# Performance work log

Hardware: AMD Instinct MI355X
Metric: run time of the kernel (lower is better)

The kernel has to match this reference:

```python
import jax, jax.numpy as jnp
import numpy as np

B, C, Z, E = 2, 32, 4, 2
N = C * C * Z  # 4096 grid points per element
P_TH, T_TH = 0.5, 0.5
ELE_D = (0.74, 0.528)


def _consts():
    real_size = jnp.array([25.0, 25.0, 3.0], jnp.float32)
    lattice = real_size / jnp.array([C, C, Z], jnp.float32)
    g = jnp.stack(jnp.meshgrid(jnp.arange(C), jnp.arange(C), jnp.arange(Z), indexing='ij'), axis=-1)
    pit = g.reshape(N, 3).astype(jnp.float32)
    return pit, lattice


def _cdist(a, b):
    # a [M,3], b [K,3] -> [M,K] euclidean distance
    d2 = jnp.sum((a[:, None, :] - b[None, :, :]) ** 2, axis=-1)
    return jnp.sqrt(d2)


def _nms(pos, conf, valid, ele_d):
    # Fixed-shape version of Analyzer.nms: sort by confidence desc (invalid -> -inf, sorts last),
    # triu(<d) adjacency restricted to valid points, matrix-multiply suppression correction.
    key = jnp.where(valid, conf, -jnp.inf)
    order = jnp.argsort(-key)              # descending confidence
    pos_s = pos[order]
    valid_s = valid[order]
    dist = _cdist(pos_s, pos_s)            # [N,N] ~ 64 MB
    iu = jnp.triu(jnp.ones((N, N), bool), k=1)
    adj = ((dist < ele_d) & iu & valid_s[:, None] & valid_s[None, :]).astype(pos.dtype)
    restrain = adj.sum(0)                  # col sums: # earlier neighbors
    restrain_one = (restrain != 0).astype(pos.dtype)
    correct = restrain_one @ adj           # earlier neighbors that are themselves suppressed
    sel = ((restrain - correct) == 0) & valid_s
    keep = jnp.zeros(N, bool).at[order].set(sel)
    return keep & valid


def _match(t_pos, t_valid, p_pos, p_valid, ele_d):
    # TP matching: T point is matched if any valid P within ele_d; argmin gives its P partner.
    dist = _cdist(t_pos, p_pos)            # [N,N]
    dist = jnp.where(t_valid[:, None] & p_valid[None, :], dist, jnp.inf)
    tp_t_mask = (dist < ele_d).any(1)      # rows in torch's TP_T_index
    tp_p_idx = jnp.argmin(dist, axis=1).astype(jnp.int32)  # torch's TP_P_index (valid where tp_t_mask)
    return tp_t_mask, tp_p_idx


def setup_inputs() -> dict:
    key = jax.random.key(0)
    k1, k2 = jax.random.split(key)
    predictions = jax.random.uniform(k1, (B, C, C, Z, E, 4), jnp.float32)
    targets = jax.random.uniform(k2, (B, C, C, Z, E, 4), jnp.float32)
    return {"predictions": predictions, "targets": targets}


def reference(predictions, targets):
    pit, lattice = _consts()
    # [B,C,C,Z,E,4] -> [B,E,N,4]
    pred = predictions.reshape(B, C, C, Z, E, 4).transpose(0, 4, 1, 2, 3, 5).reshape(B, E, N, 4)
    tgt = targets.reshape(B, C, C, Z, E, 4).transpose(0, 4, 1, 2, 3, 5).reshape(B, E, N, 4)

    p_pos = (pred[..., :3] + pit) * lattice    # [B,E,N,3] absolute coords
    p_conf = pred[..., 3]
    mask_p = p_conf > P_TH
    t_pos = (tgt[..., :3] + pit) * lattice
    mask_t = tgt[..., 3] > T_TH

    keeps, tpt, tpp, tptn, tppn = [], [], [], [], []
    for e in range(E):
        d = ELE_D[e]
        keep_e = jax.vmap(lambda p, c, v: _nms(p, c, v, d))(p_pos[:, e], p_conf[:, e], mask_p[:, e])
        tt, tp = jax.vmap(lambda tq, tv, pq, pv: _match(tq, tv, pq, pv, d))(
            t_pos[:, e], mask_t[:, e], p_pos[:, e], mask_p[:, e])
        ttn, tpn = jax.vmap(lambda tq, tv, pq, pv: _match(tq, tv, pq, pv, d))(
            t_pos[:, e], mask_t[:, e], p_pos[:, e], keep_e)
        keeps.append(keep_e); tpt.append(tt); tpp.append(tp); tptn.append(ttn); tppn.append(tpn)

    keep_nms = jnp.stack(keeps, 1)   # [B,E,N] combined mask_p & nms keep
    tp_t_mask = jnp.stack(tpt, 1)
    tp_p_idx = jnp.stack(tpp, 1)
    tp_t_mask_nms = jnp.stack(tptn, 1)
    tp_p_idx_nms = jnp.stack(tppn, 1)

    return (p_pos, mask_p, keep_nms, t_pos, mask_t,
            tp_t_mask, tp_p_idx, tp_t_mask_nms, tp_p_idx_nms)
```

## Files before the change

### kernel.cpp

```cpp
#include <hip/hip_runtime.h>
#include <cmath>
#include <cstdint>

namespace {
constexpr int NPT  = 4096;

constexpr int O_PPOS  = 0;
constexpr int O_MASKP = 49152;
constexpr int O_KEEP  = 65536;
constexpr int O_TPOS  = 81920;
constexpr int O_MASKT = 131072;
constexpr int O_TPT   = 147456;
constexpr int O_TPP   = 163840;
constexpr int O_TPTN  = 180224;
constexpr int O_TPPN  = 196608;

constexpr float GUARD = 1.4999f;
}

__device__ __forceinline__ unsigned long long shfl_xor_u64(unsigned long long v, int m) {
    unsigned lo = (unsigned)v, hi = (unsigned)(v >> 32);
    lo = __shfl_xor(lo, m); hi = __shfl_xor(hi, m);
    return ((unsigned long long)hi << 32) | lo;
}

__device__ __forceinline__ float3 cellpos(float4 p, int n) {
#pragma clang fp contract(off)
    float fx = (float)(n >> 7), fy = (float)((n >> 2) & 31), fz = (float)(n & 3);
    float3 r;
    r.x = (p.x + fx) * 0.78125f;
    r.y = (p.y + fy) * 0.78125f;
    r.z = (p.z + fz) * 0.75f;
    return r;
}
__device__ __forceinline__ float dist2(float3 a, float3 b) {
#pragma clang fp contract(off)
    float dx = a.x - b.x, dy = a.y - b.y, dz = a.z - b.z;
    float d2 = dx * dx + dy * dy;
    return d2 + dz * dz;
}

__global__ void __launch_bounds__(256) k_nms(const float4* __restrict__ pred,
                                             float* __restrict__ out,
                                             unsigned char* __restrict__ keepu,
                                             float s0, float s1) {
#pragma clang fp contract(off)
    __shared__ unsigned char restr[216];
    int bid = blockIdx.x;
    int h2 = bid & 1, gx = (bid >> 1) & 31, s = bid >> 6;
    int b = s >> 1, e = s & 1;
    int base4 = b * 8192 + e;
    float se = (s & 1) ? s1 : s0;
    int gy0 = h2 << 4;
    int t = (int)threadIdx.x;

    if (t < 216) {
        int rgx = t / 72, rem = t - rgx * 72, rgy = rem >> 2, z = rem & 3;
        int px = gx + rgx - 1, py = gy0 + rgy - 1;
        unsigned c = 0;
        if ((unsigned)px < 32u && (unsigned)py < 32u) {
            int pn = px * 128 + py * 4 + z;
            float4 p = pred[base4 + pn * 2];
            if (p.w > 0.5f) {
                float3 pj = cellpos(p, pn);
                for (int q = 0; q < 9; ++q) {
                    int nx = px + q / 3 - 1, ny = py + q % 3 - 1;
                    if ((unsigned)nx > 31u || (unsigned)ny > 31u) continue;
                    int nb = nx * 128 + ny * 4;
#pragma unroll
                    for (int nz = 0; nz < 4; ++nz) {
                        int ni = nb + nz;
                        float4 pi = pred[base4 + ni * 2];
                        float3 qi = cellpos(pi, ni);
                        float d2 = dist2(pj, qi);
                        bool prec = (pi.w > p.w) || ((pi.w == p.w) && (ni < pn));
                        if ((pi.w > 0.5f) && (d2 < se) && prec) c++;
                    }
                }
            }
        }
        restr[t] = (unsigned char)c;
    }
    __syncthreads();

    int r = t >> 2, h = t & 3;
    int gy = gy0 + (r >> 2), z = r & 3;
    int n = (gx << 7) + (gy << 2) + z;
    int row = s * NPT + n;
    float4 p = pred[base4 + n * 2];
    float3 pj = cellpos(p, n);
    bool valid = p.w > 0.5f;
    unsigned any = 0;
    if (valid) {
        for (int qq = 0; qq < 3; ++qq) {
            int q = qq * 4 + h;
            if (q > 8) continue;
            int dx = q / 3 - 1, dy = q % 3 - 1;
            int nx = gx + dx, ny = gy + dy;
            if ((unsigned)nx > 31u || (unsigned)ny > 31u) continue;
            int nb = nx * 128 + ny * 4;
            const unsigned char* lr = &restr[(dx + 1) * 72 + (gy - gy0 + dy + 1) * 4];
#pragma unroll
            for (int nz = 0; nz < 4; ++nz) {
                int ni = nb + nz;
                float4 pi = pred[base4 + ni * 2];
                float3 qi = cellpos(pi, ni);
                float d2 = dist2(pj, qi);
                bool prec = (pi.w > p.w) || ((pi.w == p.w) && (ni < n));
                bool flg = (pi.w > 0.5f) && (lr[nz] == 0);
                if (flg && (d2 < se) && prec) any = 1u;
            }
        }
    }
    any |= __shfl_xor(any, 1);
    any |= __shfl_xor(any, 2);
    if (h == 0) {
        out[O_PPOS + row * 3 + 0] = pj.x;
        out[O_PPOS + row * 3 + 1] = pj.y;
        out[O_PPOS + row * 3 + 2] = pj.z;
        out[O_MASKP + row] = valid ? 1.0f : 0.0f;
        bool keep = valid && !any;
        out[O_KEEP + row] = keep ? 1.0f : 0.0f;
        keepu[row] = keep ? 1 : 0;
    }
}

__global__ void __launch_bounds__(256) k_match(const float4* __restrict__ pred,
                                               const float4* __restrict__ tgt,
                                               const unsigned char* __restrict__ keepu,
                                               float* __restrict__ out,
                                               float s0, float s1) {
#pragma clang fp contract(off)
    int tid = blockIdx.x * 256 + (int)threadIdx.x;
    int row = tid >> 2, h = tid & 3;
    int n = row & (NPT - 1), s = row >> 12, b = s >> 1, e = s & 1;
    int base4 = b * 8192 + e, srow = s * NPT;
    float se = (s & 1) ? s1 : s0;
    float4 t4 = tgt[base4 + n * 2];
    float3 tj = cellpos(t4, n);
    bool tv = t4.w > 0.5f;
    if (h == 0) {
        out[O_TPOS + row * 3 + 0] = tj.x;
        out[O_TPOS + row * 3 + 1] = tj.y;
        out[O_TPOS + row * 3 + 2] = tj.z;
        out[O_MASKT + row] = tv ? 1.0f : 0.0f;
    }
    if (!tv) {
        if (h == 0) {
            out[O_TPT + row] = 0.0f; out[O_TPTN + row] = 0.0f;
            out[O_TPP + row] = 0.0f; out[O_TPPN + row] = 0.0f;
        }
        return;
    }
    int gx = n >> 7, gy = (n >> 2) & 31;
    unsigned long long bs = ~0ull, bn = ~0ull;
    unsigned as_ = 0, an_ = 0;
    for (int qq = 0; qq < 7; ++qq) {
        int q = qq * 4 + h;
        if (q > 24) continue;
        int nx = gx + q / 5 - 2, ny = gy + q % 5 - 2;
        if ((unsigned)nx > 31u || (unsigned)ny > 31u) continue;
        int nb = nx * 128 + ny * 4;
#pragma unroll
        for (int nz = 0; nz < 4; ++nz) {
            int ni = nb + nz;
            float4 pi = pred[base4 + ni * 2];
            float3 qi = cellpos(pi, ni);
            float d2 = dist2(tj, qi);
            float dist = sqrtf(d2);
            unsigned long long enc =
                ((unsigned long long)__float_as_uint(dist) << 32) | (unsigned)ni;
            if (pi.w > 0.5f) { if (enc < bs) bs = enc; if (d2 < se) as_ = 1u; }
            if (keepu[srow + ni]) { if (enc < bn) bn = enc; if (d2 < se) an_ = 1u; }
        }
    }
    for (int m = 1; m < 4; m <<= 1) {
        unsigned long long o = shfl_xor_u64(bs, m); if (o < bs) bs = o;
        o = shfl_xor_u64(bn, m); if (o < bn) bn = o;
        as_ |= __shfl_xor(as_, m);
        an_ |= __shfl_xor(an_, m);
    }
    bool acc_s = __uint_as_float((unsigned)(bs >> 32)) < GUARD;
    bool acc_n = __uint_as_float((unsigned)(bn >> 32)) < GUARD;
    if (!(acc_s && acc_n)) {
        unsigned long long fs = ~0ull, fn = ~0ull;
        for (int k = h; k < NPT; k += 4) {
            float4 pi = pred[base4 + k * 2];
            float3 qi = cellpos(pi, k);
            float d2 = dist2(tj, qi);
            float dist = sqrtf(d2);
            unsigned long long enc =
                ((unsigned long long)__float_as_uint(dist) << 32) | (unsigned)k;
            if (pi.w > 0.5f && enc < fs) fs = enc;
            if (keepu[srow + k] && enc < fn) fn = enc;
        }
        for (int m = 1; m < 4; m <<= 1) {
            unsigned long long o = shfl_xor_u64(fs, m); if (o < fs) fs = o;
            o = shfl_xor_u64(fn, m); if (o < fn) fn = o;
        }
        bs = fs; bn = fn;
    }
    if (h == 0) {
        out[O_TPT + row]  = as_ ? 1.0f : 0.0f;
        out[O_TPTN + row] = an_ ? 1.0f : 0.0f;
        out[O_TPP + row]  = (float)((bs == ~0ull) ? 0u : (unsigned)(bs & 0xffffffffull));
        out[O_TPPN + row] = (float)((bn == ~0ull) ? 0u : (unsigned)(bn & 0xffffffffull));
    }
}

static float sq_boundary(float t) {
    float f = (float)((double)t * (double)t);
    while (sqrtf(f) >= t) f = nextafterf(f, 0.0f);
    while (sqrtf(f) < t)  f = nextafterf(f, __builtin_inff());
    return f;
}

extern "C" void kernel_launch(void* const* d_in, const int* in_sizes, int n_in,
                              void* d_out, int out_size, void* d_ws, size_t ws_size,
                              hipStream_t stream) {
    (void)in_sizes; (void)n_in; (void)out_size; (void)ws_size;
    const float4* pred = (const float4*)d_in[0];
    const float4* tgt  = (const float4*)d_in[1];
    float* out = (float*)d_out;
    unsigned char* keepu = (unsigned char*)d_ws;

    float s0 = sq_boundary(0.74f);
    float s1 = sq_boundary(0.528f);

    k_nms  <<<dim3(256), dim3(256), 0, stream>>>(pred, out, keepu, s0, s1);
    k_match<<<dim3(256), dim3(256), 0, stream>>>(pred, tgt, keepu, out, s0, s1);
}
```

Before: 75.77 us.

## Fuse NMS and matching into one kernel using halo recomputation of keep flags

Merges the NMS and matching kernels into a single launch. Each block recomputes restrain counts over a 3-cell halo and keep flags over a 2-cell halo in shared memory, so the matching step reads keep flags locally instead of through a global workspace. The rare full-scan fallback recomputes keep on demand through a noinline helper. This removes one launch and the global keep buffer round trip, at the cost of redundant halo computation and a very expensive fallback path.

```diff
diff --git a/kernel.cpp b/kernel.cpp
--- a/kernel.cpp
+++ b/kernel.cpp
@@ -40,12 +40,63 @@
     return d2 + dz * dz;
 }
 
-__global__ void __launch_bounds__(256) k_nms(const float4* __restrict__ pred,
+__device__ __forceinline__ unsigned restrain_of(const float4* __restrict__ pred,
+                                                int base4, int pn, float se) {
+#pragma clang fp contract(off)
+    float4 p = pred[base4 + pn * 2];
+    if (!(p.w > 0.5f)) return 0u;
+    float3 pj = cellpos(p, pn);
+    int gx = pn >> 7, gy = (pn >> 2) & 31;
+    unsigned c = 0;
+    for (int q = 0; q < 9; ++q) {
+        int nx = gx + q / 3 - 1, ny = gy + q % 3 - 1;
+        if ((unsigned)nx > 31u || (unsigned)ny > 31u) continue;
+        int nb = nx * 128 + ny * 4;
+#pragma unroll
+        for (int nz = 0; nz < 4; ++nz) {
+            int ni = nb + nz;
+            float4 pi = pred[base4 + ni * 2];
+            float3 qi = cellpos(pi, ni);
+            float d2 = dist2(pj, qi);
+            bool prec = (pi.w > p.w) || ((pi.w == p.w) && (ni < pn));
+            if ((pi.w > 0.5f) && (d2 < se) && prec) c++;
+        }
+    }
+    return c;
+}
+
+__device__ __noinline__ bool keep_of(const float4* __restrict__ pred,
+                                     int base4, int k, float se) {
+#pragma clang fp contract(off)
+    float4 p = pred[base4 + k * 2];
+    if (!(p.w > 0.5f)) return false;
+    float3 pj = cellpos(p, k);
+    int gx = k >> 7, gy = (k >> 2) & 31;
+    for (int q = 0; q < 9; ++q) {
+        int nx = gx + q / 3 - 1, ny = gy + q % 3 - 1;
+        if ((unsigned)nx > 31u || (unsigned)ny > 31u) continue;
+        int nb = nx * 128 + ny * 4;
+        for (int nz = 0; nz < 4; ++nz) {
+            int ni = nb + nz;
+            float4 pi = pred[base4 + ni * 2];
+            float3 qi = cellpos(pi, ni);
+            float d2 = dist2(pj, qi);
+            bool prec = (pi.w > p.w) || ((pi.w == p.w) && (ni < k));
+            if ((pi.w > 0.5f) && (d2 < se) && prec &&
+                restrain_of(pred, base4, ni, se) == 0u)
+                return false;
+        }
+    }
+    return true;
+}
+
+__global__ void __launch_bounds__(256) k_all(const float4* __restrict__ pred,
+                                             const float4* __restrict__ tgt,
                                              float* __restrict__ out,
-                                             unsigned char* __restrict__ keepu,
                                              float s0, float s1) {
 #pragma clang fp contract(off)
-    __shared__ unsigned char restr[216];
+    __shared__ unsigned char restr[7 * 22 * 4];
+    __shared__ unsigned char keepl[5 * 20 * 4];
     int bid = blockIdx.x;
     int h2 = bid & 1, gx = (bid >> 1) & 31, s = bid >> 6;
     int b = s >> 1, e = s & 1;
@@ -54,19 +105,35 @@
     int gy0 = h2 << 4;
     int t = (int)threadIdx.x;
 
-    if (t < 216) {
-        int rgx = t / 72, rem = t - rgx * 72, rgy = rem >> 2, z = rem & 3;
-        int px = gx + rgx - 1, py = gy0 + rgy - 1;
+    for (int ra = t; ra < 616; ra += 256) {
+        int rx = ra / 88, rem = ra - rx * 88, ry = rem >> 2, z = rem & 3;
+        int px = gx + rx - 3, py = gy0 + ry - 3;
         unsigned c = 0;
+        if ((unsigned)px < 32u && (unsigned)py < 32u)
+            c = restrain_of(pred, base4, px * 128 + py * 4 + z, se);
+        restr[ra] = (unsigned char)c;
+    }
+    __syncthreads();
+
+    for (int kb = t; kb < 400; kb += 256) {
+        int kx = kb / 80, rem = kb - kx * 80, ky = rem >> 2, z = rem & 3;
+        int px = gx + kx - 2, py = gy0 + ky - 2;
+        bool keep = false;
+        bool interior = (kx == 2) && (ky >= 2) && (ky < 18);
         if ((unsigned)px < 32u && (unsigned)py < 32u) {
             int pn = px * 128 + py * 4 + z;
             float4 p = pred[base4 + pn * 2];
-            if (p.w > 0.5f) {
-                float3 pj = cellpos(p, pn);
+            float3 pj = cellpos(p, pn);
+            bool valid = p.w > 0.5f;
+            unsigned any = 0;
+            if (valid) {
                 for (int q = 0; q < 9; ++q) {
-                    int nx = px + q / 3 - 1, ny = py + q % 3 - 1;
+                    int dx = q / 3 - 1, dy = q % 3 - 1;
+                    int nx = px + dx, ny = py + dy;
                     if ((unsigned)nx > 31u || (unsigned)ny > 31u) continue;
                     int nb = nx * 128 + ny * 4;
+                    const unsigned char* lr =
+                        &restr[((kx + dx + 1) * 22 + (ky + dy + 1)) * 4];
 #pragma unroll
                     for (int nz = 0; nz < 4; ++nz) {
                         int ni = nb + nz;
@@ -74,12 +141,22 @@
                         float3 qi = cellpos(pi, ni);
                         float d2 = dist2(pj, qi);
                         bool prec = (pi.w > p.w) || ((pi.w == p.w) && (ni < pn));
-                        if ((pi.w > 0.5f) && (d2 < se) && prec) c++;
+                        bool flg = (pi.w > 0.5f) && (lr[nz] == 0);
+                        if (flg && (d2 < se) && prec) any = 1u;
                     }
                 }
             }
-        }
-        restr[t] = (unsigned char)c;
+            keep = valid && !any;
+            if (interior) {
+                int row = s * NPT + pn;
+                out[O_PPOS + row * 3 + 0] = pj.x;
+                out[O_PPOS + row * 3 + 1] = pj.y;
+                out[O_PPOS + row * 3 + 2] = pj.z;
+                out[O_MASKP + row] = valid ? 1.0f : 0.0f;
+                out[O_KEEP + row] = keep ? 1.0f : 0.0f;
+            }
+        }
+        keepl[kb] = keep ? 1 : 0;
     }
     __syncthreads();
 
@@ -87,55 +164,6 @@
     int gy = gy0 + (r >> 2), z = r & 3;
     int n = (gx << 7) + (gy << 2) + z;
     int row = s * NPT + n;
-    float4 p = pred[base4 + n * 2];
-    float3 pj = cellpos(p, n);
-    bool valid = p.w > 0.5f;
-    unsigned any = 0;
-    if (valid) {
-        for (int qq = 0; qq < 3; ++qq) {
-            int q = qq * 4 + h;
-            if (q > 8) continue;
-            int dx = q / 3 - 1, dy = q % 3 - 1;
-            int nx = gx + dx, ny = gy + dy;
-            if ((unsigned)nx > 31u || (unsigned)ny > 31u) continue;
-            int nb = nx * 128 + ny * 4;
-            const unsigned char* lr = &restr[(dx + 1) * 72 + (gy - gy0 + dy + 1) * 4];
-#pragma unroll
-            for (int nz = 0; nz < 4; ++nz) {
-                int ni = nb + nz;
-                float4 pi = pred[base4 + ni * 2];
-                float3 qi = cellpos(pi, ni);
-                float d2 = dist2(pj, qi);
-                bool prec = (pi.w > p.w) || ((pi.w == p.w) && (ni < n));
-                bool flg = (pi.w > 0.5f) && (lr[nz] == 0);
-                if (flg && (d2 < se) && prec) any = 1u;
-            }
-        }
-    }
-    any |= __shfl_xor(any, 1);
-    any |= __shfl_xor(any, 2);
-    if (h == 0) {
-        out[O_PPOS + row * 3 + 0] = pj.x;
-        out[O_PPOS + row * 3 + 1] = pj.y;
-        out[O_PPOS + row * 3 + 2] = pj.z;
-        out[O_MASKP + row] = valid ? 1.0f : 0.0f;
-        bool keep = valid && !any;
-        out[O_KEEP + row] = keep ? 1.0f : 0.0f;
-        keepu[row] = keep ? 1 : 0;
-    }
-}
-
-__global__ void __launch_bounds__(256) k_match(const float4* __restrict__ pred,
-                                               const float4* __restrict__ tgt,
-                                               const unsigned char* __restrict__ keepu,
-                                               float* __restrict__ out,
-                                               float s0, float s1) {
-#pragma clang fp contract(off)
-    int tid = blockIdx.x * 256 + (int)threadIdx.x;
-    int row = tid >> 2, h = tid & 3;
-    int n = row & (NPT - 1), s = row >> 12, b = s >> 1, e = s & 1;
-    int base4 = b * 8192 + e, srow = s * NPT;
-    float se = (s & 1) ? s1 : s0;
     float4 t4 = tgt[base4 + n * 2];
     float3 tj = cellpos(t4, n);
     bool tv = t4.w > 0.5f;
@@ -152,15 +180,17 @@
         }
         return;
     }
-    int gx = n >> 7, gy = (n >> 2) & 31;
     unsigned long long bs = ~0ull, bn = ~0ull;
     unsigned as_ = 0, an_ = 0;
     for (int qq = 0; qq < 7; ++qq) {
         int q = qq * 4 + h;
         if (q > 24) continue;
-        int nx = gx + q / 5 - 2, ny = gy + q % 5 - 2;
+        int dx = q / 5 - 2, dy = q % 5 - 2;
+        int nx = gx + dx, ny = gy + dy;
         if ((unsigned)nx > 31u || (unsigned)ny > 31u) continue;
         int nb = nx * 128 + ny * 4;
+        const unsigned char* lk =
+            &keepl[((dx + 2) * 20 + (gy - gy0 + dy + 2)) * 4];
 #pragma unroll
         for (int nz = 0; nz < 4; ++nz) {
             int ni = nb + nz;
@@ -171,7 +201,7 @@
             unsigned long long enc =
                 ((unsigned long long)__float_as_uint(dist) << 32) | (unsigned)ni;
             if (pi.w > 0.5f) { if (enc < bs) bs = enc; if (d2 < se) as_ = 1u; }
-            if (keepu[srow + ni]) { if (enc < bn) bn = enc; if (d2 < se) an_ = 1u; }
+            if (lk[nz]) { if (enc < bn) bn = enc; if (d2 < se) an_ = 1u; }
         }
     }
     for (int m = 1; m < 4; m <<= 1) {
@@ -192,7 +222,7 @@
             unsigned long long enc =
                 ((unsigned long long)__float_as_uint(dist) << 32) | (unsigned)k;
             if (pi.w > 0.5f && enc < fs) fs = enc;
-            if (keepu[srow + k] && enc < fn) fn = enc;
+            if (enc < fn && keep_of(pred, base4, k, se)) fn = enc;
         }
         for (int m = 1; m < 4; m <<= 1) {
             unsigned long long o = shfl_xor_u64(fs, m); if (o < fs) fs = o;
@@ -218,15 +248,13 @@
 extern "C" void kernel_launch(void* const* d_in, const int* in_sizes, int n_in,
                               void* d_out, int out_size, void* d_ws, size_t ws_size,
                               hipStream_t stream) {
-    (void)in_sizes; (void)n_in; (void)out_size; (void)ws_size;
+    (void)in_sizes; (void)n_in; (void)out_size; (void)d_ws; (void)ws_size;
     const float4* pred = (const float4*)d_in[0];
     const float4* tgt  = (const float4*)d_in[1];
     float* out = (float*)d_out;
-    unsigned char* keepu = (unsigned char*)d_ws;
 
     float s0 = sq_boundary(0.74f);
     float s1 = sq_boundary(0.528f);
 
-    k_nms  <<<dim3(256), dim3(256), 0, stream>>>(pred, out, keepu, s0, s1);
-    k_match<<<dim3(256), dim3(256), 0, stream>>>(pred, tgt, keepu, out, s0, s1);
-}
+    k_all<<<dim3(256), dim3(256), 0, stream>>>(pred, tgt, out, s0, s1);
+}
```

Result: slower. 94.91 us (+25.3%).
